# Kernel tuning notes

Measured on AMD Instinct MI355X. Metric: run time of the kernel, lower is better.

The kernel has to match this reference:

```python
import jax, jax.numpy as jnp
import numpy as np

EPS = 1e-6  # AngularPhysicsConfig.eps


def setup_inputs() -> dict:
    key = jax.random.key(0)
    k1, k2 = jax.random.split(key)
    B, L, d, H = 2, 2048, 2048, 8
    x_spatial = jax.random.normal(k1, (B, L, d), dtype=jnp.float32)
    # attn is a softmax output: rows sum to 1 over the last axis
    attn = jax.nn.softmax(jax.random.normal(k2, (B, H, L, L), dtype=jnp.float32), axis=-1)
    W = jnp.ones((1,), dtype=jnp.float32)   # nn.Parameter(torch.ones(1))
    b = jnp.zeros((1,), dtype=jnp.float32)  # bias_init = 0.0
    return {"x_spatial": x_spatial, "attn": attn, "W": W, "b": b}


def reference(x_spatial, attn, W, b):
    # --- angular_kernel ---
    norm = jnp.clip(jnp.linalg.norm(x_spatial, axis=-1, keepdims=True), EPS, None)
    x_unit = x_spatial / norm                                   # [B, L, d]
    K = jnp.einsum('bld,bmd->blm', x_unit, x_unit)              # [B, L, L] cosine sim
    K_mean = K.mean(axis=(-1, -2), keepdims=True)
    K_cent = K - K_mean
    # torch .std() is unbiased (ddof=1), computed on detached K_cent
    K_std = jnp.std(jax.lax.stop_gradient(K_cent), axis=(-1, -2), keepdims=True, ddof=1)
    K_norm = K_cent / jnp.clip(K_std, EPS, None)                # [B, L, L]

    # --- compute_cos_align (detach_attn_for_alignment=True) ---
    A = jax.lax.stop_gradient(attn.mean(axis=1))                # [B, L, L]
    cos_align = jnp.sum(A * K_norm, axis=-1)                    # [B, L]

    # --- gate ---
    gate = jax.nn.sigmoid(W * cos_align + b)                    # [B, L]
    return gate, cos_align, K_norm
```

## Files before the change

### kernel.cpp

```cpp
#include <hip/hip_runtime.h>
#include <hip/hip_bf16.h>

#define L_DIM 2048
#define D_DIM 2048
#define B_DIM 2
#define H_DIM 8
#define EPSV 1e-6f

using bf16x8 = __attribute__((ext_vector_type(8))) __bf16;
using f32x4  = __attribute__((ext_vector_type(4))) float;

__device__ inline void gload_lds16(const void* g, void* l) {
    __builtin_amdgcn_global_load_lds(
        (const __attribute__((address_space(1))) void*)g,
        (__attribute__((address_space(3))) void*)l, 16, 0, 0);
}

__device__ inline ushort f2bf(float f) {
    unsigned int u = __float_as_uint(f);
    unsigned int lsb = (u >> 16) & 1u;
    u += 0x7fffu + lsb;
    return (ushort)(u >> 16);
}

__global__ __launch_bounds__(256) void k_normalize(const float* __restrict__ x,
                                                   ushort* __restrict__ xu,
                                                   double* __restrict__ sums) {
    const int row = blockIdx.x;
    const int t   = threadIdx.x;
    const float* xr = x + (size_t)row * D_DIM;
    float4 v0 = ((const float4*)xr)[t];
    float4 v1 = ((const float4*)xr)[t + 256];
    float ss = v0.x*v0.x + v0.y*v0.y + v0.z*v0.z + v0.w*v0.w
             + v1.x*v1.x + v1.y*v1.y + v1.z*v1.z + v1.w*v1.w;
    #pragma unroll
    for (int off = 32; off; off >>= 1) ss += __shfl_down(ss, off);
    __shared__ float red[4];
    __shared__ float s_inv;
    if ((t & 63) == 0) red[t >> 6] = ss;
    __syncthreads();
    if (t == 0) {
        float nrm = sqrtf(red[0] + red[1] + red[2] + red[3]);
        nrm = fmaxf(nrm, EPSV);
        s_inv = 1.0f / nrm;
    }
    __syncthreads();
    const float inv = s_inv;
    ushort* xo = xu + (size_t)row * D_DIM;
    ushort4 o0, o1;
    o0.x = f2bf(v0.x * inv); o0.y = f2bf(v0.y * inv);
    o0.z = f2bf(v0.z * inv); o0.w = f2bf(v0.w * inv);
    o1.x = f2bf(v1.x * inv); o1.y = f2bf(v1.y * inv);
    o1.z = f2bf(v1.z * inv); o1.w = f2bf(v1.w * inv);
    ((ushort4*)xo)[t]       = o0;
    ((ushort4*)xo)[t + 256] = o1;
    if (row == 0 && t < 4) sums[t] = 0.0;
}

__global__ __launch_bounds__(256) void k_gemm(const ushort* __restrict__ Xu,
                                              float* __restrict__ Kout,
                                              double* __restrict__ sums) {
    __shared__ __align__(16) ushort lds_a[128 * 32];
    __shared__ __align__(16) ushort lds_b[128 * 32];
    const int t    = threadIdx.x;
    const int lane = t & 63;
    const int w    = t >> 6;
    const int wr   = w >> 1, wc = w & 1;
    const int bRow = blockIdx.x * 128;
    const int bCol = blockIdx.y * 128;
    const int batch = blockIdx.z;
    const ushort* Xb = Xu + (size_t)batch * L_DIM * D_DIM;

    const int srow = t >> 2;
    const int scol = (t & 3) * 8;
    const ushort* gA0 = Xb + (size_t)(bRow + srow)      * D_DIM + scol;
    const ushort* gA1 = Xb + (size_t)(bRow + 64 + srow) * D_DIM + scol;
    const ushort* gB0 = Xb + (size_t)(bCol + srow)      * D_DIM + scol;
    const ushort* gB1 = Xb + (size_t)(bCol + 64 + srow) * D_DIM + scol;
    ushort* lA0 = lds_a + t * 8;
    ushort* lA1 = lds_a + 64 * 32 + t * 8;
    ushort* lB0 = lds_b + t * 8;
    ushort* lB1 = lds_b + 64 * 32 + t * 8;

    f32x4 acc[4][4] = {};
    const int frow = lane & 15;
    const int fk   = lane >> 4;

    for (int kt = 0; kt < D_DIM / 32; ++kt) {
        __syncthreads();
        const size_t ko = (size_t)kt * 32;
        gload_lds16(gA0 + ko, lA0);
        gload_lds16(gA1 + ko, lA1);
        gload_lds16(gB0 + ko, lB0);
        gload_lds16(gB1 + ko, lB1);
        __syncthreads();
        bf16x8 a[4], b[4];
        #pragma unroll
        for (int m = 0; m < 4; ++m)
            a[m] = *(const bf16x8*)&lds_a[(wr * 64 + m * 16 + frow) * 32 + fk * 8];
        #pragma unroll
        for (int n = 0; n < 4; ++n)
            b[n] = *(const bf16x8*)&lds_b[(wc * 64 + n * 16 + frow) * 32 + fk * 8];
        #pragma unroll
        for (int m = 0; m < 4; ++m)
            #pragma unroll
            for (int n = 0; n < 4; ++n)
                acc[m][n] = __builtin_amdgcn_mfma_f32_16x16x32_bf16(a[m], b[n], acc[m][n], 0, 0, 0);
    }

    float* Kb = Kout + (size_t)batch * L_DIM * L_DIM;
    float ps = 0.f, pss = 0.f;
    #pragma unroll
    for (int m = 0; m < 4; ++m) {
        #pragma unroll
        for (int n = 0; n < 4; ++n) {
            #pragma unroll
            for (int j = 0; j < 4; ++j) {
                const int r = bRow + wr * 64 + m * 16 + fk * 4 + j;
                const int c = bCol + wc * 64 + n * 16 + frow;
                const float v = acc[m][n][j];
                Kb[(size_t)r * L_DIM + c] = v;
                ps += v; pss += v * v;
            }
        }
    }
    #pragma unroll
    for (int off = 32; off; off >>= 1) {
        ps  += __shfl_down(ps, off);
        pss += __shfl_down(pss, off);
    }
    __shared__ float redS[4], redSS[4];
    if (lane == 0) { redS[w] = ps; redSS[w] = pss; }
    __syncthreads();
    if (t == 0) {
        atomicAdd(&sums[batch * 2],     (double)(redS[0] + redS[1] + redS[2] + redS[3]));
        atomicAdd(&sums[batch * 2 + 1], (double)(redSS[0] + redSS[1] + redSS[2] + redSS[3]));
    }
}

__global__ __launch_bounds__(256) void k_epilogue(const float* __restrict__ attn,
                                                  float* __restrict__ out,
                                                  const double* __restrict__ sums,
                                                  const float* __restrict__ Wp,
                                                  const float* __restrict__ bp) {
    const int row = blockIdx.x;
    const int b = row >> 11;
    const int l = row & (L_DIM - 1);
    const int t = threadIdx.x;

    const double N = (double)L_DIM * (double)L_DIM;
    const double mean_d = sums[b * 2] / N;
    double var = (sums[b * 2 + 1] - N * mean_d * mean_d) / (N - 1.0);
    var = var > 0.0 ? var : 0.0;
    float sd = (float)sqrt(var);
    sd = fmaxf(sd, EPSV);
    const float inv_std = 1.0f / sd;
    const float mean = (float)mean_d;

    float* Krow = out + 2 * B_DIM * L_DIM + ((size_t)b * L_DIM + l) * L_DIM;
    const float* abase = attn + ((size_t)b * H_DIM * L_DIM + l) * L_DIM;

    float dot = 0.f;
    #pragma unroll
    for (int it = 0; it < 2; ++it) {
        const int i = t * 4 + it * 1024;
        float4 kv = *(const float4*)&Krow[i];
        float4 kn;
        kn.x = (kv.x - mean) * inv_std;
        kn.y = (kv.y - mean) * inv_std;
        kn.z = (kv.z - mean) * inv_std;
        kn.w = (kv.w - mean) * inv_std;
        *(float4*)&Krow[i] = kn;
        float ax = 0.f, ay = 0.f, az = 0.f, aw = 0.f;
        #pragma unroll
        for (int h = 0; h < H_DIM; ++h) {
            const float4 av = *(const float4*)&abase[(size_t)h * L_DIM * L_DIM + i];
            ax += av.x; ay += av.y; az += av.z; aw += av.w;
        }
        dot += 0.125f * (ax * kn.x + ay * kn.y + az * kn.z + aw * kn.w);
    }
    #pragma unroll
    for (int off = 32; off; off >>= 1) dot += __shfl_down(dot, off);
    __shared__ float red[4];
    if ((t & 63) == 0) red[t >> 6] = dot;
    __syncthreads();
    if (t == 0) {
        const float ca = red[0] + red[1] + red[2] + red[3];
        out[B_DIM * L_DIM + row] = ca;
        const float z = Wp[0] * ca + bp[0];
        out[row] = 1.0f / (1.0f + expf(-z));
    }
}

extern "C" void kernel_launch(void* const* d_in, const int* in_sizes, int n_in,
                              void* d_out, int out_size, void* d_ws, size_t ws_size,
                              hipStream_t stream) {
    const float* x    = (const float*)d_in[0];
    const float* attn = (const float*)d_in[1];
    const float* W    = (const float*)d_in[2];
    const float* bb   = (const float*)d_in[3];
    float* out = (float*)d_out;

    ushort* xu   = (ushort*)d_ws;
    double* sums = (double*)((char*)d_ws + (size_t)B_DIM * L_DIM * D_DIM * 2);
    float*  Kbuf = out + 2 * B_DIM * L_DIM;

    hipLaunchKernelGGL(k_normalize, dim3(B_DIM * L_DIM), dim3(256), 0, stream, x, xu, sums);
    hipLaunchKernelGGL(k_gemm, dim3(L_DIM / 128, L_DIM / 128, B_DIM), dim3(256), 0, stream,
                       xu, Kbuf, sums);
    hipLaunchKernelGGL(k_epilogue, dim3(B_DIM * L_DIM), dim3(256), 0, stream,
                       attn, out, sums, W, bb);
}
```

Baseline: 130.2 us.

## Fuse attention-weighted row dot into GEMM epilogue using softmax row-sum identity

The head-mean attention dot product moves out of the epilogue kernel and into the GEMM kernel. Each GEMM block reads its tile of attn across all heads and dots it with the raw K tile it just wrote, then float-atomically accumulates per-row partials into the cos_align slot. The epilogue then recovers cos_align as (dot - mean)/std, which is valid only because attn rows sum to 1 (softmax), and keeps only the K normalization pass. The aim is to overlap the large attn stream with other blocks' MFMA work and to re-read K while it is likely still in cache. The cost is per-row float atomics, which make results order-dependent, and a dependence on the softmax row-sum property.

```diff
diff --git a/kernel.cpp b/kernel.cpp
--- a/kernel.cpp
+++ b/kernel.cpp
@@ -25,7 +25,8 @@
 
 __global__ __launch_bounds__(256) void k_normalize(const float* __restrict__ x,
                                                    ushort* __restrict__ xu,
-                                                   double* __restrict__ sums) {
+                                                   double* __restrict__ sums,
+                                                   float* __restrict__ dotacc) {
     const int row = blockIdx.x;
     const int t   = threadIdx.x;
     const float* xr = x + (size_t)row * D_DIM;
@@ -43,6 +44,8 @@
         float nrm = sqrtf(red[0] + red[1] + red[2] + red[3]);
         nrm = fmaxf(nrm, EPSV);
         s_inv = 1.0f / nrm;
+        dotacc[row] = 0.0f;
+        if (row == 0) { sums[0] = 0.0; sums[1] = 0.0; sums[2] = 0.0; sums[3] = 0.0; }
     }
     __syncthreads();
     const float inv = s_inv;
@@ -54,12 +57,13 @@
     o1.z = f2bf(v1.z * inv); o1.w = f2bf(v1.w * inv);
     ((ushort4*)xo)[t]       = o0;
     ((ushort4*)xo)[t + 256] = o1;
-    if (row == 0 && t < 4) sums[t] = 0.0;
 }
 
 __global__ __launch_bounds__(256) void k_gemm(const ushort* __restrict__ Xu,
+                                              const float* __restrict__ attn,
                                               float* __restrict__ Kout,
-                                              double* __restrict__ sums) {
+                                              double* __restrict__ sums,
+                                              float* __restrict__ dotacc) {
     __shared__ __align__(16) ushort lds_a[128 * 32];
     __shared__ __align__(16) ushort lds_b[128 * 32];
     const int t    = threadIdx.x;
@@ -136,16 +140,35 @@
         atomicAdd(&sums[batch * 2],     (double)(redS[0] + redS[1] + redS[2] + redS[3]));
         atomicAdd(&sums[batch * 2 + 1], (double)(redSS[0] + redSS[1] + redSS[2] + redSS[3]));
     }
-}
-
-__global__ __launch_bounds__(256) void k_epilogue(const float* __restrict__ attn,
-                                                  float* __restrict__ out,
+
+    const float* ab = attn + (size_t)batch * H_DIM * L_DIM * L_DIM;
+    const int g  = t >> 5;
+    const int cc = (t & 31) * 4;
+    #pragma unroll 2
+    for (int i = 0; i < 16; ++i) {
+        const int r = i * 8 + g;
+        const size_t roff = (size_t)(bRow + r) * L_DIM + (bCol + cc);
+        float4 s = {0.f, 0.f, 0.f, 0.f};
+        #pragma unroll
+        for (int h = 0; h < H_DIM; ++h) {
+            const float4 av = *(const float4*)(ab + (size_t)h * L_DIM * L_DIM + roff);
+            s.x += av.x; s.y += av.y; s.z += av.z; s.w += av.w;
+        }
+        const float4 kv = *(const float4*)&Kb[roff];
+        float v = s.x * kv.x + s.y * kv.y + s.z * kv.z + s.w * kv.w;
+        #pragma unroll
+        for (int off = 16; off; off >>= 1) v += __shfl_down(v, off, 32);
+        if ((t & 31) == 0)
+            atomicAdd(&dotacc[batch * L_DIM + bRow + r], 0.125f * v);
+    }
+}
+
+__global__ __launch_bounds__(256) void k_epilogue(float* __restrict__ out,
                                                   const double* __restrict__ sums,
                                                   const float* __restrict__ Wp,
                                                   const float* __restrict__ bp) {
     const int row = blockIdx.x;
     const int b = row >> 11;
-    const int l = row & (L_DIM - 1);
     const int t = threadIdx.x;
 
     const double N = (double)L_DIM * (double)L_DIM;
@@ -157,10 +180,7 @@
     const float inv_std = 1.0f / sd;
     const float mean = (float)mean_d;
 
-    float* Krow = out + 2 * B_DIM * L_DIM + ((size_t)b * L_DIM + l) * L_DIM;
-    const float* abase = attn + ((size_t)b * H_DIM * L_DIM + l) * L_DIM;
-
-    float dot = 0.f;
+    float* Krow = out + 2 * B_DIM * L_DIM + (size_t)row * L_DIM;
     #pragma unroll
     for (int it = 0; it < 2; ++it) {
         const int i = t * 4 + it * 1024;
@@ -171,21 +191,10 @@
         kn.z = (kv.z - mean) * inv_std;
         kn.w = (kv.w - mean) * inv_std;
         *(float4*)&Krow[i] = kn;
-        float ax = 0.f, ay = 0.f, az = 0.f, aw = 0.f;
-        #pragma unroll
-        for (int h = 0; h < H_DIM; ++h) {
-            const float4 av = *(const float4*)&abase[(size_t)h * L_DIM * L_DIM + i];
-            ax += av.x; ay += av.y; az += av.z; aw += av.w;
-        }
-        dot += 0.125f * (ax * kn.x + ay * kn.y + az * kn.z + aw * kn.w);
-    }
-    #pragma unroll
-    for (int off = 32; off; off >>= 1) dot += __shfl_down(dot, off);
-    __shared__ float red[4];
-    if ((t & 63) == 0) red[t >> 6] = dot;
-    __syncthreads();
+    }
     if (t == 0) {
-        const float ca = red[0] + red[1] + red[2] + red[3];
+        const float dotv = out[B_DIM * L_DIM + row];
+        const float ca = (dotv - mean) * inv_std;
         out[B_DIM * L_DIM + row] = ca;
         const float z = Wp[0] * ca + bp[0];
         out[row] = 1.0f / (1.0f + expf(-z));
@@ -204,10 +213,12 @@
     ushort* xu   = (ushort*)d_ws;
     double* sums = (double*)((char*)d_ws + (size_t)B_DIM * L_DIM * D_DIM * 2);
     float*  Kbuf = out + 2 * B_DIM * L_DIM;
-
-    hipLaunchKernelGGL(k_normalize, dim3(B_DIM * L_DIM), dim3(256), 0, stream, x, xu, sums);
+    float*  dotacc = out + B_DIM * L_DIM;
+
+    hipLaunchKernelGGL(k_normalize, dim3(B_DIM * L_DIM), dim3(256), 0, stream,
+                       x, xu, sums, dotacc);
     hipLaunchKernelGGL(k_gemm, dim3(L_DIM / 128, L_DIM / 128, B_DIM), dim3(256), 0, stream,
-                       xu, Kbuf, sums);
+                       xu, attn, Kbuf, sums, dotacc);
     hipLaunchKernelGGL(k_epilogue, dim3(B_DIM * L_DIM), dim3(256), 0, stream,
-                       attn, out, sums, W, bb);
-}
+                       out, sums, W, bb);
+}
```

Result: no change. 131.2 us (+0.7%).
